# Performance work log

Hardware: AMD Instinct MI355X
Metric: run time of the kernel (lower is better)

Reference implementation:

```python
import jax, jax.numpy as jnp
import numpy as np

N, H, E, K, C, M = 4096, 512, 512, 64, 128, 4  # tokens, hidden, embed, categories, children/cat, max_num_children
IN = E + H  # LSTMCell input size


def setup_inputs() -> dict:
    key = jax.random.key(0)
    ks = jax.random.split(key, 12)
    s = 0.05
    return {
        "et": jax.random.normal(ks[0], (N, H), jnp.float32),
        "x": jax.random.normal(ks[1], (N, IN), jnp.float32),
        "h": jax.random.normal(ks[2], (N, H), jnp.float32),
        "c": jax.random.normal(ks[3], (N, H), jnp.float32),
        "cat": jax.random.randint(ks[4], (N,), 0, K, jnp.int32),
        "ci": jax.random.randint(ks[5], (N,), 0, M, jnp.int32),
        # per-category prediction Linear(hidden_size -> |children(category)|)
        "W_lin": jax.random.normal(ks[6], (K, C, H), jnp.float32) * s,
        "b_lin": jax.random.normal(ks[7], (K, C), jnp.float32) * s,
        # per-child-index LSTMCell(embedding+hidden -> hidden), torch gate order i,f,g,o
        "W_ih": jax.random.normal(ks[8], (M, 4 * H, IN), jnp.float32) * s,
        "W_hh": jax.random.normal(ks[9], (M, 4 * H, H), jnp.float32) * s,
        "b_ih": jax.random.normal(ks[10], (M, 4 * H), jnp.float32) * s,
        "b_hh": jax.random.normal(ks[11], (M, 4 * H), jnp.float32) * s,
    }


def reference(et, x, h, c, cat, ci, W_lin, b_lin, W_ih, W_hh, b_ih, b_hh):
    # get_log_odds: route each token to its category's Linear (gather weights, per-token matvec)
    Wg = W_lin[cat]                                   # [N, C, H]
    log_odds = jnp.einsum('nh,nch->nc', et, Wg) + b_lin[cat]  # [N, C]

    # get_next: LSTMCell selected by child_index. Only M=4 cells, so compute all
    # cells' gates densely (efficient GEMMs) and select with a one-hot mix.
    gates_all = (jnp.einsum('ni,kgi->nkg', x, W_ih)
                 + jnp.einsum('nh,kgh->nkg', h, W_hh)
                 + (b_ih + b_hh)[None])               # [N, M, 4H]
    sel = jax.nn.one_hot(ci, M, dtype=gates_all.dtype)  # [N, M]
    gates = jnp.einsum('nkg,nk->ng', gates_all, sel)     # [N, 4H]
    i_, f_, g_, o_ = jnp.split(gates, 4, axis=-1)
    c2 = jax.nn.sigmoid(f_) * c + jax.nn.sigmoid(i_) * jnp.tanh(g_)
    h2 = jax.nn.sigmoid(o_) * jnp.tanh(c2)
    return log_odds, h2, c2
```

## Files before the change

### kernel.cpp

```cpp
#include <hip/hip_runtime.h>
#include <hip/hip_bf16.h>
#include <stdint.h>

#define NTOK 4096
#define HID  512
#define INSZ 1024
#define KIN  1536
#define KSEG 768
#define KCAT 64
#define CCH  128
#define MCELL 4
#define G4H  2048
#define AROWS 5120

typedef unsigned short u16;
typedef __bf16 bf16x8 __attribute__((ext_vector_type(8)));
typedef float  f32x4  __attribute__((ext_vector_type(4)));

__device__ __forceinline__ u16 f2bf(float f) {
    unsigned u = __float_as_uint(f);
    u += 0x7fffu + ((u >> 16) & 1u);
    return (u16)(u >> 16);
}
__device__ __forceinline__ float bf2f(u16 v) {
    return __uint_as_float(((unsigned)v) << 16);
}
__device__ __forceinline__ void store_bf8(u16* p, float4 a, float4 b) {
    ushort4 r0, r1;
    r0.x = f2bf(a.x); r0.y = f2bf(a.y); r0.z = f2bf(a.z); r0.w = f2bf(a.w);
    r1.x = f2bf(b.x); r1.y = f2bf(b.y); r1.z = f2bf(b.z); r1.w = f2bf(b.w);
    *reinterpret_cast<ushort4*>(p) = r0;
    *reinterpret_cast<ushort4*>(p + 4) = r1;
}
__device__ __forceinline__ void gl16(const u16* g, u16* l) {
    __builtin_amdgcn_global_load_lds((const __attribute__((address_space(1))) void*)g,
                                     (__attribute__((address_space(3))) void*)l, 16, 0, 0);
}

__global__ __launch_bounds__(1024) void build_perm(
    const int* __restrict__ ci, const int* __restrict__ cat,
    int* __restrict__ meta, int* __restrict__ perm_ci,
    int* __restrict__ inv_ci, int* __restrict__ perm_cat)
{
    __shared__ int cnt_ci[MCELL], cur_ci[MCELL];
    __shared__ int cnt_cat[KCAT], cur_cat[KCAT];
    int tid = threadIdx.x;
    if (tid < MCELL) cnt_ci[tid] = 0;
    if (tid < KCAT)  cnt_cat[tid] = 0;
    __syncthreads();
    for (int t = tid; t < NTOK; t += 1024) {
        atomicAdd(&cnt_ci[ci[t]], 1);
        atomicAdd(&cnt_cat[cat[t]], 1);
    }
    __syncthreads();
    if (tid == 0) {
        int off = 0;
        for (int m = 0; m < MCELL; ++m) {
            int p = (cnt_ci[m] + 255) & ~255;
            meta[m] = p; meta[4 + m] = off; cur_ci[m] = off; off += p;
        }
        off = 0;
        for (int i = 0; i < 128; ++i) meta[136 + i] = -1;
        for (int k = 0; k < KCAT; ++k) {
            int p = (cnt_cat[k] + 63) & ~63;
            meta[8 + k] = p; meta[72 + k] = off; cur_cat[k] = off;
            for (int i = 0; i < p / 64; ++i) meta[136 + off / 64 + i] = k;
            off += p;
        }
    }
    __syncthreads();
    for (int i = tid; i < AROWS; i += 1024) perm_ci[i] = -1;
    for (int i = tid; i < 8192; i += 1024) perm_cat[i] = -1;
    __syncthreads();
    for (int t = tid; t < NTOK; t += 1024) {
        int s = atomicAdd(&cur_ci[ci[t]], 1);
        perm_ci[s] = t;
        inv_ci[t] = s;
        int sc = atomicAdd(&cur_cat[cat[t]], 1);
        perm_cat[sc] = t;
    }
}

#define CH_W  (8192 * 192)
#define CH_L  (8192 * 64)
#define CH_A  (AROWS * 192)
#define CH_TOT (CH_W + CH_L + CH_A)
#define PK_BLOCKS 2048

__global__ __launch_bounds__(256) void fat_pack(
    const float* __restrict__ x, const float* __restrict__ h,
    const float* __restrict__ Wih, const float* __restrict__ Whh,
    const float* __restrict__ W_lin,
    const int* __restrict__ perm_ci,
    u16* __restrict__ A_pack, u16* __restrict__ Wb, u16* __restrict__ Wlin)
{
    for (int i = blockIdx.x * 256 + threadIdx.x; i < CH_TOT; i += PK_BLOCKS * 256) {
        if (i < CH_W) {
            int row = i / 192, cc = i - row * 192;
            int m = row >> 11, j = row & 2047;
            int c = cc * 8;
            const float* src = (c < INSZ) ? (Wih + ((size_t)m * G4H + j) * INSZ + c)
                                          : (Whh + ((size_t)m * G4H + j) * HID + (c - INSZ));
            store_bf8(Wb + (size_t)row * KIN + c,
                      *(const float4*)src, *(const float4*)(src + 4));
        } else if (i < CH_W + CH_L) {
            int i2 = i - CH_W;
            int row = i2 >> 6, cc = i2 & 63;
            const float* src = W_lin + (size_t)row * HID + cc * 8;
            store_bf8(Wlin + (size_t)row * HID + cc * 8,
                      *(const float4*)src, *(const float4*)(src + 4));
        } else {
            int i3 = i - (CH_W + CH_L);
            int row = i3 / 192, cc = i3 - row * 192;
            int c = cc * 8;
            u16* dst = A_pack + (size_t)row * KIN + c;
            int t = perm_ci[row];
            if (t < 0) {
                *reinterpret_cast<int4*>(dst) = make_int4(0, 0, 0, 0);
            } else {
                const float* src = (c < INSZ) ? (x + (size_t)t * INSZ + c)
                                              : (h + (size_t)t * HID + (c - INSZ));
                store_bf8(dst, *(const float4*)src, *(const float4*)(src + 4));
            }
        }
    }
}

__global__ __launch_bounds__(256, 2) void mega_gemm(
    const u16* __restrict__ A_pack,
    const u16* __restrict__ Wb,
    const u16* __restrict__ Wlin,
    const float* __restrict__ et,
    const float* __restrict__ b_lin,
    const int* __restrict__ meta,
    const int* __restrict__ perm_cat,
    u16* __restrict__ gates0,
    u16* __restrict__ gates1,
    float* __restrict__ out)
{
    __shared__ __align__(16) u16 As[16384];
    __shared__ __align__(16) u16 Bs[8192];
    __shared__ int sperm[64];

    int tid = threadIdx.x;
    int lane = tid & 63, wave = tid >> 6;
    int qd = lane >> 4, l15 = lane & 15;
    int rsw = l15 & 7;

    int id = blockIdx.x;
    if (id < 1280) {
        int g = id & 63;
        int r = id >> 6;
        int m = g >> 4, ct = g & 15;
        int seg = r & 1, rt = r >> 1;
        int pcnt = meta[m];
        if (rt * 256 >= pcnt) return;
        int row0 = meta[4 + m] + rt * 256;
        int k0 = seg * KSEG;

        const u16* gA[8]; const u16* gB[4];
        u16* lA[8]; u16* lB[4];
        #pragma unroll
        for (int j = 0; j < 8; ++j) {
            int q = j * 256 + wave * 64 + lane;
            int row = q >> 3, kc = (q & 7) ^ (row & 7);
            gA[j] = A_pack + (size_t)(row0 + row) * KIN + k0 + kc * 8;
            lA[j] = As + q * 8;
        }
        #pragma unroll
        for (int j = 0; j < 4; ++j) {
            int q = j * 256 + wave * 64 + lane;
            int row = q >> 3, kc = (q & 7) ^ (row & 7);
            gB[j] = Wb + ((size_t)m * G4H + ct * 128 + row) * KIN + k0 + kc * 8;
            lB[j] = Bs + q * 8;
        }

        int wm = wave >> 1, wn = wave & 1;

        f32x4 acc[8][4];
        #pragma unroll
        for (int i = 0; i < 8; ++i)
            #pragma unroll
            for (int j = 0; j < 4; ++j)
                acc[i][j] = (f32x4){0.f, 0.f, 0.f, 0.f};

        for (int ks = 0; ks < KSEG / 64; ++ks) {
            #pragma unroll
            for (int j = 0; j < 8; ++j) { gl16(gA[j], lA[j]); gA[j] += 64; }
            #pragma unroll
            for (int j = 0; j < 4; ++j) { gl16(gB[j], lB[j]); gB[j] += 64; }
            __syncthreads();
            #pragma unroll
            for (int ks2 = 0; ks2 < 2; ++ks2) {
                int ch = (ks2 * 4 + qd) ^ rsw;
                bf16x8 fb[4];
                #pragma unroll
                for (int tj = 0; tj < 4; ++tj) {
                    int row = wn * 64 + tj * 16 + l15;
                    fb[tj] = *reinterpret_cast<const bf16x8*>(&Bs[row * 64 + ch * 8]);
                }
                #pragma unroll
                for (int ti = 0; ti < 8; ++ti) {
                    int row = wm * 128 + ti * 16 + l15;
                    bf16x8 fa = *reinterpret_cast<const bf16x8*>(&As[row * 64 + ch * 8]);
                    #pragma unroll
                    for (int tj = 0; tj < 4; ++tj)
                        acc[ti][tj] = __builtin_amdgcn_mfma_f32_16x16x32_bf16(fa, fb[tj], acc[ti][tj], 0, 0, 0);
                }
            }
            __syncthreads();
        }

        u16* gout = seg ? gates1 : gates0;
        #pragma unroll
        for (int ti = 0; ti < 8; ++ti) {
            #pragma unroll
            for (int tj = 0; tj < 4; ++tj) {
                int gcol = ct * 128 + wn * 64 + tj * 16 + l15;
                #pragma unroll
                for (int rr = 0; rr < 4; ++rr) {
                    int grow = row0 + wm * 128 + ti * 16 + qd * 4 + rr;
                    gout[(size_t)grow * G4H + gcol] = f2bf(acc[ti][tj][rr]);
                }
            }
        }
    } else {
        int rtl = id - 1280;
        int k = meta[136 + rtl];
        if (k < 0) return;
        int r0 = rtl * 64;

        if (tid < 64) sperm[tid] = perm_cat[r0 + tid];
        __syncthreads();

        int rb = tid >> 3;
        int kc = (tid & 7) ^ (rb & 7);

        const u16* gW[4]; u16* lW[4];
        #pragma unroll
        for (int i = 0; i < 4; ++i) {
            gW[i] = Wlin + ((size_t)k * CCH + i * 32 + rb) * HID + kc * 8;
            lW[i] = As + (i * 256 + wave * 64) * 8;
        }
        int ar = tid >> 2;
        int acp = tid & 3;
        int at = sperm[ar];
        const float* asrc = (at >= 0) ? (et + (size_t)at * HID) : nullptr;

        f32x4 acc[4][2];
        #pragma unroll
        for (int i = 0; i < 4; ++i) {
            acc[i][0] = (f32x4){0.f, 0.f, 0.f, 0.f};
            acc[i][1] = (f32x4){0.f, 0.f, 0.f, 0.f};
        }

        for (int kk = 0; kk < HID; kk += 64) {
            #pragma unroll
            for (int i = 0; i < 4; ++i) { gl16(gW[i], lW[i]); gW[i] += 64; }
            #pragma unroll
            for (int j = 0; j < 2; ++j) {
                int dch = acp * 2 + j;
                int sch = dch ^ (ar & 7);
                u16* dst = &Bs[ar * 64 + dch * 8];
                if (asrc) {
                    const float* s = asrc + kk + sch * 8;
                    store_bf8(dst, *(const float4*)s, *(const float4*)(s + 4));
                } else {
                    *reinterpret_cast<int4*>(dst) = make_int4(0, 0, 0, 0);
                }
            }
            __syncthreads();
            #pragma unroll
            for (int ks2 = 0; ks2 < 2; ++ks2) {
                int ch = (ks2 * 4 + qd) ^ rsw;
                bf16x8 fa[4], fb[2];
                #pragma unroll
                for (int ti = 0; ti < 4; ++ti)
                    fa[ti] = *reinterpret_cast<const bf16x8*>(&Bs[(ti * 16 + l15) * 64 + ch * 8]);
                #pragma unroll
                for (int tj = 0; tj < 2; ++tj)
                    fb[tj] = *reinterpret_cast<const bf16x8*>(&As[(wave * 32 + tj * 16 + l15) * 64 + ch * 8]);
                #pragma unroll
                for (int ti = 0; ti < 4; ++ti)
                    #pragma unroll
                    for (int tj = 0; tj < 2; ++tj)
                        acc[ti][tj] = __builtin_amdgcn_mfma_f32_16x16x32_bf16(fa[ti], fb[tj], acc[ti][tj], 0, 0, 0);
            }
            __syncthreads();
        }

        #pragma unroll
        for (int ti = 0; ti < 4; ++ti) {
            #pragma unroll
            for (int tj = 0; tj < 2; ++tj) {
                int n = wave * 32 + tj * 16 + l15;
                float bias = b_lin[k * CCH + n];
                #pragma unroll
                for (int rr = 0; rr < 4; ++rr) {
                    int row = ti * 16 + qd * 4 + rr;
                    int t = sperm[row];
                    if (t >= 0)
                        out[(size_t)t * CCH + n] = acc[ti][tj][rr] + bias;
                }
            }
        }
    }
}

__global__ __launch_bounds__(256) void lstm_epilogue(
    const u16* __restrict__ gates0, const u16* __restrict__ gates1,
    const int* __restrict__ meta,
    const int* __restrict__ inv_ci,
    const float* __restrict__ c,
    const float* __restrict__ b_ih,
    const float* __restrict__ b_hh,
    float* __restrict__ out)
{
    int idx = blockIdx.x * 256 + threadIdx.x;
    int t = idx >> 9;
    int hh = idx & 511;
    int s = inv_ci[t];
    int m = (s >= meta[5]) + (s >= meta[6]) + (s >= meta[7]);

    const u16* g0 = gates0 + (size_t)s * G4H;
    const u16* g1 = gates1 + (size_t)s * G4H;
    const float* bi = b_ih + (size_t)m * G4H;
    const float* bh = b_hh + (size_t)m * G4H;
    float gi = bf2f(g0[hh])        + bf2f(g1[hh])        + bi[hh]        + bh[hh];
    float gf = bf2f(g0[512 + hh])  + bf2f(g1[512 + hh])  + bi[512 + hh]  + bh[512 + hh];
    float gg = bf2f(g0[1024 + hh]) + bf2f(g1[1024 + hh]) + bi[1024 + hh] + bh[1024 + hh];
    float go = bf2f(g0[1536 + hh]) + bf2f(g1[1536 + hh]) + bi[1536 + hh] + bh[1536 + hh];

    float si = 1.f / (1.f + __expf(-gi));
    float sf = 1.f / (1.f + __expf(-gf));
    float so = 1.f / (1.f + __expf(-go));
    float ct = c[(size_t)t * HID + hh];
    float c2 = sf * ct + si * tanhf(gg);
    float h2 = so * tanhf(c2);

    const size_t o_h2 = (size_t)NTOK * CCH;
    const size_t o_c2 = o_h2 + (size_t)NTOK * HID;
    out[o_h2 + (size_t)t * HID + hh] = h2;
    out[o_c2 + (size_t)t * HID + hh] = c2;
}

extern "C" void kernel_launch(void* const* d_in, const int* in_sizes, int n_in,
                              void* d_out, int out_size, void* d_ws, size_t ws_size,
                              hipStream_t stream) {
    const float* et    = (const float*)d_in[0];
    const float* x     = (const float*)d_in[1];
    const float* h     = (const float*)d_in[2];
    const float* c     = (const float*)d_in[3];
    const int*   cat   = (const int*)d_in[4];
    const int*   ci    = (const int*)d_in[5];
    const float* W_lin = (const float*)d_in[6];
    const float* b_lin = (const float*)d_in[7];
    const float* W_ih  = (const float*)d_in[8];
    const float* W_hh  = (const float*)d_in[9];
    const float* b_ih  = (const float*)d_in[10];
    const float* b_hh  = (const float*)d_in[11];
    float* out = (float*)d_out;

    char* ws = (char*)d_ws;
    int* meta     = (int*)ws;
    int* perm_ci  = (int*)(ws + 2048);
    int* perm_cat = (int*)(ws + 22528);
    int* inv_ci   = (int*)(ws + 55296);
    u16* A_pack   = (u16*)(ws + 71680);
    u16* Wb       = (u16*)(ws + 15800320);
    u16* Wlin     = (u16*)(ws + 40966144);
    u16* gates0   = (u16*)(ws + 49354752);
    u16* gates1   = (u16*)(ws + 70326272);

    build_perm<<<1, 1024, 0, stream>>>(ci, cat, meta, perm_ci, inv_ci, perm_cat);

    fat_pack<<<PK_BLOCKS, 256, 0, stream>>>(x, h, W_ih, W_hh, W_lin, perm_ci,
                                            A_pack, Wb, Wlin);

    mega_gemm<<<1280 + 128, 256, 0, stream>>>(A_pack, Wb, Wlin, et, b_lin, meta,
                                              perm_cat, gates0, gates1, out);

    lstm_epilogue<<<(NTOK * HID) / 256, 256, 0, stream>>>(gates0, gates1, meta,
                                                          inv_ci, c, b_ih, b_hh, out);
}
```

Measured before the change: 236.1 us.

## Use 512-thread blocks with smaller per-wave tiles and schedule category blocks first

The fused GEMM kernel now launches 512-thread blocks. Each of eight waves computes a 64x64 sub-tile of the 256x128 LSTM gate tile instead of 128x64, which halves the accumulator registers per wave, and launch bounds target four blocks per CU. The small per-category Linear blocks are moved to the front of the grid so they no longer trail behind the large GEMM blocks. Cooperative loads are reindexed for 512 threads. The trade-off is less register-level reuse per wave and more LDS fragment reads relative to MFMA work, in exchange for more waves to hide latency.

```diff
diff --git a/kernel.cpp b/kernel.cpp
--- a/kernel.cpp
+++ b/kernel.cpp
@@ -126,7 +126,7 @@
     }
 }
 
-__global__ __launch_bounds__(256, 2) void mega_gemm(
+__global__ __launch_bounds__(512, 4) void mega_gemm(
     const u16* __restrict__ A_pack,
     const u16* __restrict__ Wb,
     const u16* __restrict__ Wlin,
@@ -148,9 +148,10 @@
     int rsw = l15 & 7;
 
     int id = blockIdx.x;
-    if (id < 1280) {
-        int g = id & 63;
-        int r = id >> 6;
+    if (id >= 128) {
+        int id2 = id - 128;
+        int g = id2 & 63;
+        int r = id2 >> 6;
         int m = g >> 4, ct = g & 15;
         int seg = r & 1, rt = r >> 1;
         int pcnt = meta[m];
@@ -158,18 +159,18 @@
         int row0 = meta[4 + m] + rt * 256;
         int k0 = seg * KSEG;
 
-        const u16* gA[8]; const u16* gB[4];
-        u16* lA[8]; u16* lB[4];
-        #pragma unroll
-        for (int j = 0; j < 8; ++j) {
-            int q = j * 256 + wave * 64 + lane;
+        const u16* gA[4]; u16* lA[4];
+        #pragma unroll
+        for (int j = 0; j < 4; ++j) {
+            int q = j * 512 + tid;
             int row = q >> 3, kc = (q & 7) ^ (row & 7);
             gA[j] = A_pack + (size_t)(row0 + row) * KIN + k0 + kc * 8;
             lA[j] = As + q * 8;
         }
-        #pragma unroll
-        for (int j = 0; j < 4; ++j) {
-            int q = j * 256 + wave * 64 + lane;
+        const u16* gB[2]; u16* lB[2];
+        #pragma unroll
+        for (int j = 0; j < 2; ++j) {
+            int q = j * 512 + tid;
             int row = q >> 3, kc = (q & 7) ^ (row & 7);
             gB[j] = Wb + ((size_t)m * G4H + ct * 128 + row) * KIN + k0 + kc * 8;
             lB[j] = Bs + q * 8;
@@ -177,18 +178,18 @@
 
         int wm = wave >> 1, wn = wave & 1;
 
-        f32x4 acc[8][4];
-        #pragma unroll
-        for (int i = 0; i < 8; ++i)
+        f32x4 acc[4][4];
+        #pragma unroll
+        for (int i = 0; i < 4; ++i)
             #pragma unroll
             for (int j = 0; j < 4; ++j)
                 acc[i][j] = (f32x4){0.f, 0.f, 0.f, 0.f};
 
         for (int ks = 0; ks < KSEG / 64; ++ks) {
             #pragma unroll
-            for (int j = 0; j < 8; ++j) { gl16(gA[j], lA[j]); gA[j] += 64; }
-            #pragma unroll
-            for (int j = 0; j < 4; ++j) { gl16(gB[j], lB[j]); gB[j] += 64; }
+            for (int j = 0; j < 4; ++j) { gl16(gA[j], lA[j]); gA[j] += 64; }
+            #pragma unroll
+            for (int j = 0; j < 2; ++j) { gl16(gB[j], lB[j]); gB[j] += 64; }
             __syncthreads();
             #pragma unroll
             for (int ks2 = 0; ks2 < 2; ++ks2) {
@@ -200,8 +201,8 @@
                     fb[tj] = *reinterpret_cast<const bf16x8*>(&Bs[row * 64 + ch * 8]);
                 }
                 #pragma unroll
-                for (int ti = 0; ti < 8; ++ti) {
-                    int row = wm * 128 + ti * 16 + l15;
+                for (int ti = 0; ti < 4; ++ti) {
+                    int row = wm * 64 + ti * 16 + l15;
                     bf16x8 fa = *reinterpret_cast<const bf16x8*>(&As[row * 64 + ch * 8]);
                     #pragma unroll
                     for (int tj = 0; tj < 4; ++tj)
@@ -213,19 +214,19 @@
 
         u16* gout = seg ? gates1 : gates0;
         #pragma unroll
-        for (int ti = 0; ti < 8; ++ti) {
+        for (int ti = 0; ti < 4; ++ti) {
             #pragma unroll
             for (int tj = 0; tj < 4; ++tj) {
                 int gcol = ct * 128 + wn * 64 + tj * 16 + l15;
                 #pragma unroll
                 for (int rr = 0; rr < 4; ++rr) {
-                    int grow = row0 + wm * 128 + ti * 16 + qd * 4 + rr;
+                    int grow = row0 + wm * 64 + ti * 16 + qd * 4 + rr;
                     gout[(size_t)grow * G4H + gcol] = f2bf(acc[ti][tj][rr]);
                 }
             }
         }
     } else {
-        int rtl = id - 1280;
+        int rtl = id;
         int k = meta[136 + rtl];
         if (k < 0) return;
         int r0 = rtl * 64;
@@ -233,55 +234,51 @@
         if (tid < 64) sperm[tid] = perm_cat[r0 + tid];
         __syncthreads();
 
-        int rb = tid >> 3;
-        int kc = (tid & 7) ^ (rb & 7);
-
-        const u16* gW[4]; u16* lW[4];
-        #pragma unroll
-        for (int i = 0; i < 4; ++i) {
-            gW[i] = Wlin + ((size_t)k * CCH + i * 32 + rb) * HID + kc * 8;
-            lW[i] = As + (i * 256 + wave * 64) * 8;
-        }
-        int ar = tid >> 2;
-        int acp = tid & 3;
+        const u16* gW[2]; u16* lW[2];
+        #pragma unroll
+        for (int j = 0; j < 2; ++j) {
+            int q = j * 512 + tid;
+            int row = q >> 3, kc = (q & 7) ^ (row & 7);
+            gW[j] = Wlin + ((size_t)k * CCH + row) * HID + kc * 8;
+            lW[j] = As + q * 8;
+        }
+        int ar = tid >> 3;
+        int sch = (tid & 7) ^ (ar & 7);
         int at = sperm[ar];
         const float* asrc = (at >= 0) ? (et + (size_t)at * HID) : nullptr;
-
-        f32x4 acc[4][2];
-        #pragma unroll
-        for (int i = 0; i < 4; ++i) {
+        u16* adst = Bs + tid * 8;
+
+        int wm2 = wave & 1, wn2 = wave >> 1;
+
+        f32x4 acc[2][2];
+        #pragma unroll
+        for (int i = 0; i < 2; ++i) {
             acc[i][0] = (f32x4){0.f, 0.f, 0.f, 0.f};
             acc[i][1] = (f32x4){0.f, 0.f, 0.f, 0.f};
         }
 
         for (int kk = 0; kk < HID; kk += 64) {
             #pragma unroll
-            for (int i = 0; i < 4; ++i) { gl16(gW[i], lW[i]); gW[i] += 64; }
-            #pragma unroll
-            for (int j = 0; j < 2; ++j) {
-                int dch = acp * 2 + j;
-                int sch = dch ^ (ar & 7);
-                u16* dst = &Bs[ar * 64 + dch * 8];
-                if (asrc) {
-                    const float* s = asrc + kk + sch * 8;
-                    store_bf8(dst, *(const float4*)s, *(const float4*)(s + 4));
-                } else {
-                    *reinterpret_cast<int4*>(dst) = make_int4(0, 0, 0, 0);
-                }
+            for (int j = 0; j < 2; ++j) { gl16(gW[j], lW[j]); gW[j] += 64; }
+            if (asrc) {
+                const float* s = asrc + kk + sch * 8;
+                store_bf8(adst, *(const float4*)s, *(const float4*)(s + 4));
+            } else {
+                *reinterpret_cast<int4*>(adst) = make_int4(0, 0, 0, 0);
             }
             __syncthreads();
             #pragma unroll
             for (int ks2 = 0; ks2 < 2; ++ks2) {
                 int ch = (ks2 * 4 + qd) ^ rsw;
-                bf16x8 fa[4], fb[2];
-                #pragma unroll
-                for (int ti = 0; ti < 4; ++ti)
-                    fa[ti] = *reinterpret_cast<const bf16x8*>(&Bs[(ti * 16 + l15) * 64 + ch * 8]);
+                bf16x8 fa[2], fb[2];
+                #pragma unroll
+                for (int ti = 0; ti < 2; ++ti)
+                    fa[ti] = *reinterpret_cast<const bf16x8*>(&Bs[(wm2 * 32 + ti * 16 + l15) * 64 + ch * 8]);
                 #pragma unroll
                 for (int tj = 0; tj < 2; ++tj)
-                    fb[tj] = *reinterpret_cast<const bf16x8*>(&As[(wave * 32 + tj * 16 + l15) * 64 + ch * 8]);
-                #pragma unroll
-                for (int ti = 0; ti < 4; ++ti)
+                    fb[tj] = *reinterpret_cast<const bf16x8*>(&As[(wn2 * 32 + tj * 16 + l15) * 64 + ch * 8]);
+                #pragma unroll
+                for (int ti = 0; ti < 2; ++ti)
                     #pragma unroll
                     for (int tj = 0; tj < 2; ++tj)
                         acc[ti][tj] = __builtin_amdgcn_mfma_f32_16x16x32_bf16(fa[ti], fb[tj], acc[ti][tj], 0, 0, 0);
@@ -290,14 +287,14 @@
         }
 
         #pragma unroll
-        for (int ti = 0; ti < 4; ++ti) {
+        for (int ti = 0; ti < 2; ++ti) {
             #pragma unroll
             for (int tj = 0; tj < 2; ++tj) {
-                int n = wave * 32 + tj * 16 + l15;
+                int n = wn2 * 32 + tj * 16 + l15;
                 float bias = b_lin[k * CCH + n];
                 #pragma unroll
                 for (int rr = 0; rr < 4; ++rr) {
-                    int row = ti * 16 + qd * 4 + rr;
+                    int row = wm2 * 32 + ti * 16 + qd * 4 + rr;
                     int t = sperm[row];
                     if (t >= 0)
                         out[(size_t)t * CCH + n] = acc[ti][tj][rr] + bias;
@@ -377,7 +374,7 @@
     fat_pack<<<PK_BLOCKS, 256, 0, stream>>>(x, h, W_ih, W_hh, W_lin, perm_ci,
                                             A_pack, Wb, Wlin);
 
-    mega_gemm<<<1280 + 128, 256, 0, stream>>>(A_pack, Wb, Wlin, et, b_lin, meta,
+    mega_gemm<<<128 + 1280, 512, 0, stream>>>(A_pack, Wb, Wlin, et, b_lin, meta,
                                               perm_cat, gates0, gates1, out);
 
     lstm_epilogue<<<(NTOK * HID) / 256, 256, 0, stream>>>(gates0, gates1, meta,
```

New measurement: 266.3 us. +12.8%, slower.
